# Kernel tuning notes

Hardware: AMD Instinct MI355X
Metric: run time of the kernel (lower is better)

Reference implementation:

```python
import jax, jax.numpy as jnp
import numpy as np


def setup_inputs() -> dict:
    key = jax.random.key(0)
    k1, k2 = jax.random.split(key)
    visual_features = jax.random.normal(k1, (16, 1024, 768), dtype=jnp.float32)
    text_tokens = jax.random.normal(k2, (16, 256, 768), dtype=jnp.float32)
    return {"visual_features": visual_features, "text_tokens": text_tokens, "k": 16}


def reference(visual_features, text_tokens, k):
    B, N, D = visual_features.shape
    T = min(k, N)

    # normalize (note: norm + 1e-6 in denominator, matching torch code)
    vis_norm = visual_features / (jnp.linalg.norm(visual_features, axis=-1, keepdims=True) + 1e-6)
    vis_norm = vis_norm.astype(jnp.float32)
    txt_norm = text_tokens / (jnp.linalg.norm(text_tokens, axis=-1, keepdims=True) + 1e-6)
    txt_norm = txt_norm.astype(jnp.float32)

    similarity = jnp.einsum('bnd,bmd->bnm', vis_norm, vis_norm)          # (B,N,N)
    relevance = jnp.einsum('bnd,btd->bnt', vis_norm, txt_norm).max(-1)    # (B,N)
    r_min = relevance.min(axis=1, keepdims=True)
    r_max = relevance.max(axis=1, keepdims=True)
    relevance = (relevance - r_min + 1e-6) / (r_max - r_min + 1e-6)

    kernel = relevance[:, :, None] * similarity * relevance[:, None, :]   # (B,N,N)

    di2s0 = jnp.diagonal(kernel, axis1=1, axis2=2)                        # (B,N)
    cis0 = jnp.zeros((T, B, N), dtype=kernel.dtype)
    barange = jnp.arange(B)

    def step(carry, i):
        di2s, cis = carry
        safe = jnp.maximum(di2s, 1e-12)
        j = jnp.argmax(safe, axis=-1)                                     # (B,)
        k_j = jnp.take_along_axis(kernel, j[:, None, None], axis=1)[:, 0, :]  # (B,N)
        dj = jnp.take_along_axis(di2s, j[:, None], axis=1)[:, 0]          # (B,)
        denom = jnp.sqrt(jnp.maximum(dj, 1e-12))[:, None] + 1e-8          # (B,1)
        # cis rows >= i are zero, so full-T contraction equals contraction over :i
        c_tb = jnp.take_along_axis(cis, j[None, :, None], axis=2)[:, :, 0]  # (T,B)
        cov = jnp.einsum('tb,tbn->bn', c_tb, cis)                         # (B,N)
        eis = (k_j - cov) / denom                                         # (B,N)
        cis = jax.lax.dynamic_update_index_in_dim(cis, eis, i, axis=0)
        di2s = di2s - eis ** 2
        di2s = di2s.at[barange, j].set(-jnp.inf)
        return (di2s, cis), j

    (_, _), sel = jax.lax.scan(step, (di2s0, cis0), jnp.arange(T))        # sel: (T,B)
    select_idx = jnp.sort(sel.T, axis=1)                                  # (B,T)
    selected = jnp.take_along_axis(visual_features, select_idx[:, :, None], axis=1)  # (B,T,D)
    if T < k:
        pad = jnp.zeros((B, k - T, D), dtype=selected.dtype)
        selected = jnp.concatenate([selected, pad], axis=1)
    return selected
```

## Files before the change

### kernel.cpp

```cpp
#include <hip/hip_runtime.h>
#include <math.h>

#define NB 16
#define NN 1024
#define ND 768
#define NT 256
#define NSEL 16
#define NC 64

typedef __attribute__((ext_vector_type(8))) short short8;
typedef __attribute__((ext_vector_type(4))) float f32x4;
typedef __attribute__((ext_vector_type(8))) unsigned short ushort8v;
typedef unsigned long long u64;

__device__ __align__(16) float g_invv[NB*NN];
__device__ __align__(16) float g_diagv[NB*NN];
__device__ __align__(16) float g_mrawp[NB*NN*2];
__device__ __align__(16) ushort8v g_tf[NB*2*24*2*8*64];

__device__ __forceinline__ unsigned short f2bf(float x) {
    unsigned u = __float_as_uint(x);
    return (unsigned short)((u + 0x7FFFu + ((u >> 16) & 1u)) >> 16);
}
__device__ __forceinline__ float bf2f(unsigned short h) {
    return __uint_as_float(((unsigned)h) << 16);
}
__device__ __forceinline__ size_t tfidx(int b, int th, int s, int h, int ct, int lane) {
    return ((((size_t)(b*2 + th)*24 + s)*2 + h)*8 + ct)*64 + lane;
}

__global__ __launch_bounds__(256) void ktxt(const float* __restrict__ txt) {
    int gw = (blockIdx.x * 256 + threadIdx.x) >> 6;
    int l  = threadIdx.x & 63;
    int b  = gw >> 8, r = gw & 255;
    int th = r >> 7, ct = (r >> 4) & 7, rlo = r & 15;
    const float* row = txt + (size_t)gw * ND;

    float4 x0 = *(const float4*)(row + 8*l);
    float4 y0 = *(const float4*)(row + 8*l + 4);
    float4 x1 = {0,0,0,0}, y1 = {0,0,0,0};
    bool two = (l < 32);
    if (two) {
        x1 = *(const float4*)(row + 512 + 8*l);
        y1 = *(const float4*)(row + 512 + 8*l + 4);
    }
    float s = x0.x*x0.x + x0.y*x0.y + x0.z*x0.z + x0.w*x0.w
            + y0.x*y0.x + y0.y*y0.y + y0.z*y0.z + y0.w*y0.w;
    if (two) s += x1.x*x1.x + x1.y*x1.y + x1.z*x1.z + x1.w*x1.w
                + y1.x*y1.x + y1.y*y1.y + y1.z*y1.z + y1.w*y1.w;
    #pragma unroll
    for (int off = 32; off; off >>= 1) s += __shfl_xor(s, off);
    float inv = 1.0f / (sqrtf(s) + 1e-6f);

    int kslot = l & 3;
    int lane  = kslot*16 + rlo;
    {
        int st = l >> 2;
        float a[8] = {x0.x, x0.y, x0.z, x0.w, y0.x, y0.y, y0.z, y0.w};
        ushort8v hh, ll;
        #pragma unroll
        for (int j = 0; j < 8; j++) {
            float v = a[j] * inv;
            hh[j] = f2bf(v);
            ll[j] = f2bf(v - bf2f(hh[j]));
        }
        g_tf[tfidx(b, th, st, 0, ct, lane)] = hh;
        g_tf[tfidx(b, th, st, 1, ct, lane)] = ll;
    }
    if (two) {
        int st = 16 + (l >> 2);
        float a[8] = {x1.x, x1.y, x1.z, x1.w, y1.x, y1.y, y1.z, y1.w};
        ushort8v hh, ll;
        #pragma unroll
        for (int j = 0; j < 8; j++) {
            float v = a[j] * inv;
            hh[j] = f2bf(v);
            ll[j] = f2bf(v - bf2f(hh[j]));
        }
        g_tf[tfidx(b, th, st, 0, ct, lane)] = hh;
        g_tf[tfidx(b, th, st, 1, ct, lane)] = ll;
    }
}

__global__ __launch_bounds__(256, 1) void krel(const float* __restrict__ vis) {
    int bid = blockIdx.x;
    int lid = (bid & 7) * 32 + (bid >> 3);
    int b   = lid >> 4;
    int r   = lid & 15;
    int mt  = r >> 1;
    int th  = r & 1;
    int t   = threadIdx.x;
    int w   = t >> 6, l = t & 63;

    f32x4 acc0[8], acc1[8];
    #pragma unroll
    for (int ct = 0; ct < 8; ct++) {
        acc0[ct] = (f32x4){0.f, 0.f, 0.f, 0.f};
        acc1[ct] = (f32x4){0.f, 0.f, 0.f, 0.f};
    }

    int base = mt*128 + w*32;
    const float* Ap0 = vis + ((size_t)(b*NN + base + (l & 15)))*ND + (l >> 4)*8;
    const float* Ap1 = Ap0 + (size_t)16*ND;

    const ushort8v* Bb = g_tf + (size_t)(b*2 + th)*(24*2*8*64) + l;

    float4 a0x = *(const float4*)(Ap0);
    float4 a0y = *(const float4*)(Ap0 + 4);
    float4 a1x = *(const float4*)(Ap1);
    float4 a1y = *(const float4*)(Ap1 + 4);
    float ss0 = 0.f, ss1 = 0.f;

    #define CONV8(AX, AY, AH, AL, SS)                                          \
        {                                                                      \
            float av_[8] = {AX.x, AX.y, AX.z, AX.w, AY.x, AY.y, AY.z, AY.w};   \
            ushort8v hh_, ll_;                                                 \
            _Pragma("unroll")                                                  \
            for (int j = 0; j < 8; j++) {                                      \
                hh_[j] = f2bf(av_[j]);                                         \
                ll_[j] = f2bf(av_[j] - bf2f(hh_[j]));                          \
                SS = fmaf(av_[j], av_[j], SS);                                 \
            }                                                                  \
            AH = *(short8*)&hh_;                                               \
            AL = *(short8*)&ll_;                                               \
        }

    #define MM(ACC, AA, BB)                                                    \
        _Pragma("unroll")                                                      \
        for (int ct = 0; ct < 8; ct++)                                         \
            ACC[ct] = __builtin_amdgcn_mfma_f32_16x16x32_bf16(                 \
                AA, *(short8*)&BB[ct], ACC[ct], 0, 0, 0);

    for (int s = 0; s < 24; s++) {
        const ushort8v* Bs = Bb + (size_t)s*(2*8*64);
        ushort8v bh[8], blv[8];
        #pragma unroll
        for (int ct = 0; ct < 8; ct++) {
            bh[ct]  = Bs[ct*64];
            blv[ct] = Bs[(8 + ct)*64];
        }
        float4 n0x, n0y, n1x, n1y;
        if (s < 23) {
            int k1 = (s + 1) * 32;
            n0x = *(const float4*)(Ap0 + k1);
            n0y = *(const float4*)(Ap0 + k1 + 4);
            n1x = *(const float4*)(Ap1 + k1);
            n1y = *(const float4*)(Ap1 + k1 + 4);
        }
        short8 ah0, al0, ah1, al1;
        CONV8(a0x, a0y, ah0, al0, ss0);
        CONV8(a1x, a1y, ah1, al1, ss1);
        MM(acc0, ah0, bh)  MM(acc0, al0, bh)  MM(acc0, ah0, blv)  MM(acc0, al0, blv)
        MM(acc1, ah1, bh)  MM(acc1, al1, bh)  MM(acc1, ah1, blv)  MM(acc1, al1, blv)
        if (s < 23) { a0x = n0x; a0y = n0y; a1x = n1x; a1y = n1y; }
        __builtin_amdgcn_s_barrier();
    }
    #undef MM
    #undef CONV8

    #define EPI(ACC, MOFF, SS)                                                 \
        {                                                                      \
            _Pragma("unroll")                                                  \
            for (int rr = 0; rr < 4; rr++) {                                   \
                float mx_ = ACC[0][rr];                                        \
                _Pragma("unroll")                                              \
                for (int ct = 1; ct < 8; ct++) mx_ = fmaxf(mx_, ACC[ct][rr]);  \
                _Pragma("unroll")                                              \
                for (int off = 1; off <= 8; off <<= 1)                         \
                    mx_ = fmaxf(mx_, __shfl_xor(mx_, off));                    \
                if ((l & 15) == 0)                                             \
                    g_mrawp[(size_t)(b*NN + base + (MOFF) + (l >> 4)*4 + rr)*2 + th] = mx_; \
            }                                                                  \
            float sst_ = SS;                                                   \
            sst_ += __shfl_xor(sst_, 16);                                      \
            sst_ += __shfl_xor(sst_, 32);                                      \
            if (th == 0 && l < 16) {                                           \
                int row_ = base + (MOFF) + l;                                  \
                float nrm_ = sqrtf(sst_);                                      \
                float inv_ = 1.0f / (nrm_ + 1e-6f);                            \
                g_invv[b*NN + row_] = inv_;                                    \
                float dd_ = nrm_ * inv_;                                       \
                g_diagv[b*NN + row_] = dd_ * dd_;                              \
            }                                                                  \
        }
    EPI(acc0, 0,  ss0)
    EPI(acc1, 16, ss1)
    #undef EPI
}

__global__ __launch_bounds__(1024) void kfinal(const float* __restrict__ vis,
                                               float* __restrict__ out) {
    int b = blockIdx.x;
    int t = threadIdx.x;
    int w = t >> 6, l = t & 63;

    __shared__ u64   s_key[NN];
    __shared__ float s_reln[NN];
    __shared__ __align__(16) unsigned short Chi[NC][392], Clo[NC][392];
    __shared__ float s_S[NC*65];
    __shared__ int   s_sel[NSEL], s_srt[NSEL];
    __shared__ float s_mn[16], s_mx[16], s_b2[2];

    float m0 = g_mrawp[(size_t)(b*NN + t)*2 + 0];
    float m1 = g_mrawp[(size_t)(b*NN + t)*2 + 1];
    float iv = g_invv[b*NN + t], dd = g_diagv[b*NN + t];
    float rr = fmaxf(m0, m1) * iv;
    float lmin = rr, lmax = rr;
    #pragma unroll
    for (int off = 32; off; off >>= 1) {
        lmin = fminf(lmin, __shfl_xor(lmin, off));
        lmax = fmaxf(lmax, __shfl_xor(lmax, off));
    }
    if (l == 0) { s_mn[w] = lmin; s_mx[w] = lmax; }
    __syncthreads();
    if (t == 0) {
        float mn = s_mn[0], mx = s_mx[0];
        #pragma unroll
        for (int q = 1; q < 16; q++) { mn = fminf(mn, s_mn[q]); mx = fmaxf(mx, s_mx[q]); }
        s_b2[0] = mn; s_b2[1] = mx;
    }
    __syncthreads();
    float mn = s_b2[0], mx = s_b2[1];
    float den = mx - mn + 1e-6f;
    float rn = (rr - mn + 1e-6f) / den;
    float d0 = rn * rn * dd;
    s_reln[t] = rn;
    u64 kreg = ((u64)(~__float_as_uint(d0)) << 10) | (unsigned)t;

    #pragma unroll
    for (int k = 2; k <= 64; k <<= 1) {
        #pragma unroll
        for (int j = k >> 1; j > 0; j >>= 1) {
            u64 part = __shfl_xor(kreg, j);
            bool takeMin = ((l & k) == 0) == ((l & j) == 0);
            kreg = takeMin ? (kreg < part ? kreg : part) : (kreg < part ? part : kreg);
        }
    }
    #pragma unroll
    for (int rnd = 0; rnd < 4; rnd++) {
        int dstp = 8 >> rnd;
        s_key[w*64 + l] = kreg;
        __syncthreads();
        u64 other = s_key[(w ^ dstp)*64 + (63 - l)];
        u64 m = (kreg < other) ? kreg : other;
        #pragma unroll
        for (int j = 32; j > 0; j >>= 1) {
            u64 part = __shfl_xor(m, j);
            bool takeMin = ((l & j) == 0);
            m = takeMin ? (m < part ? m : part) : (m < part ? part : m);
        }
        kreg = m;
        __syncthreads();
    }

    int   gid = (int)(kreg & 1023u);
    float d0v = __uint_as_float(~(unsigned)(kreg >> 10));

    f32x4 acc = (f32x4){0.f, 0.f, 0.f, 0.f};
    int ar0 = (w >> 2) * 16, bc0 = (w & 3) * 16;
    int cr  = (w << 2) + (l >> 4);
    int sgid = __shfl(gid, cr);
    float sc = g_invv[b*NN + sgid];
    const float* srcrow = vis + (size_t)(b*NN + sgid)*ND + (l & 15)*24;

    for (int c = 0; c < 2; c++) {
        __syncthreads();
        int kb = (l & 15) * 24;
        #pragma unroll
        for (int q = 0; q < 3; q++) {
            float4 x = *(const float4*)(srcrow + c*384 + q*8);
            float4 y = *(const float4*)(srcrow + c*384 + q*8 + 4);
            float av[8] = {x.x, x.y, x.z, x.w, y.x, y.y, y.z, y.w};
            ushort8v hh, ll;
            #pragma unroll
            for (int j = 0; j < 8; j++) {
                float vv = av[j] * sc;
                hh[j] = f2bf(vv);
                ll[j] = f2bf(vv - bf2f(hh[j]));
            }
            *(ushort8v*)&Chi[cr][kb + q*8] = hh;
            *(ushort8v*)&Clo[cr][kb + q*8] = ll;
        }
        __syncthreads();
        #pragma unroll
        for (int ks = 0; ks < 12; ks++) {
            int ko = ks*32 + (l >> 4)*8;
            short8 ah = *(const short8*)&Chi[ar0 + (l & 15)][ko];
            short8 al = *(const short8*)&Clo[ar0 + (l & 15)][ko];
            short8 bh = *(const short8*)&Chi[bc0 + (l & 15)][ko];
            short8 bl = *(const short8*)&Clo[bc0 + (l & 15)][ko];
            acc = __builtin_amdgcn_mfma_f32_16x16x32_bf16(ah, bh, acc, 0, 0, 0);
            acc = __builtin_amdgcn_mfma_f32_16x16x32_bf16(al, bh, acc, 0, 0, 0);
            acc = __builtin_amdgcn_mfma_f32_16x16x32_bf16(ah, bl, acc, 0, 0, 0);
            acc = __builtin_amdgcn_mfma_f32_16x16x32_bf16(al, bl, acc, 0, 0, 0);
        }
    }
    #pragma unroll
    for (int r = 0; r < 4; r++)
        s_S[(ar0 + (l >> 4)*4 + r)*65 + bc0 + (l & 15)] = acc[r];
    __syncthreads();

    if (w == 0) {
        float di  = d0v;
        int   gd  = gid;
        float rel = s_reln[gid];
        float ownc[NSEL];
        #pragma unroll
        for (int i = 0; i < NSEL; i++) {
            float vq = fmaxf(di, 1e-12f);
            int   gq = gd;
            int   cq = l;
            #pragma unroll
            for (int off = 32; off; off >>= 1) {
                float vo = __shfl_xor(vq, off);
                int   go = __shfl_xor(gq, off);
                int   co = __shfl_xor(cq, off);
                if (vo > vq || (vo == vq && go < gq)) { vq = vo; gq = go; cq = co; }
            }
            float dj   = __shfl(di, cq);
            float relj = __shfl(rel, cq);
            float denom = sqrtf(fmaxf(dj, 1e-12f)) + 1e-8f;
            if (l == 0) s_sel[i] = gq;

            float cov = 0.f;
            #pragma unroll
            for (int q = 0; q < i; q++)
                cov = fmaf(ownc[q], __shfl(ownc[q], cq), cov);

            float sim = s_S[l*65 + cq];
            float kj  = rel * relj * sim;
            float eis = (kj - cov) / denom;
            ownc[i] = eis;
            di = di - eis * eis;
            if (l == cq) di = -__builtin_inff();
        }
    }
    __syncthreads();

    if (t == 0) {
        int vv[16];
        #pragma unroll
        for (int q = 0; q < 16; q++) vv[q] = s_sel[q];
        for (int a = 1; a < 16; a++) {
            int key = vv[a]; int p2 = a - 1;
            while (p2 >= 0 && vv[p2] > key) { vv[p2+1] = vv[p2]; p2--; }
            vv[p2+1] = key;
        }
        #pragma unroll
        for (int q = 0; q < 16; q++) s_srt[q] = vv[q];
    }
    __syncthreads();
    {
        int idx = s_srt[w];
        const float* src = vis + (size_t)(b*NN + idx)*ND + l*12;
        float*       dst = out + (size_t)(b*NSEL + w)*ND + l*12;
        float4 x = *(const float4*)(src);
        float4 y = *(const float4*)(src + 4);
        float4 z = *(const float4*)(src + 8);
        *(float4*)(dst)     = x;
        *(float4*)(dst + 4) = y;
        *(float4*)(dst + 8) = z;
    }
}

extern "C" void kernel_launch(void* const* d_in, const int* in_sizes, int n_in,
                              void* d_out, int out_size, void* d_ws, size_t ws_size,
                              hipStream_t stream) {
    (void)in_sizes; (void)n_in; (void)d_ws; (void)ws_size; (void)out_size;
    const float* vis = (const float*)d_in[0];
    const float* txt = (const float*)d_in[1];
    float* out = (float*)d_out;

    ktxt  <<<dim3((NB*NT)/4), dim3(256),  0, stream>>>(txt);
    krel  <<<dim3(256),       dim3(256),  0, stream>>>(vis);
    kfinal<<<dim3(NB),        dim3(1024), 0, stream>>>(vis, out);
}
```

Before: 82.00 us.

## Stage B fragments in LDS via async triple-buffered loads in krel

Result: slower. 88.52 us (+8.0%).

```diff
diff --git a/kernel.cpp b/kernel.cpp
--- a/kernel.cpp
+++ b/kernel.cpp
@@ -82,15 +82,17 @@
     }
 }
 
-__global__ __launch_bounds__(256, 1) void krel(const float* __restrict__ vis) {
+__global__ __launch_bounds__(128, 1) void krel(const float* __restrict__ vis) {
     int bid = blockIdx.x;
-    int lid = (bid & 7) * 32 + (bid >> 3);
-    int b   = lid >> 4;
-    int r   = lid & 15;
-    int mt  = r >> 1;
+    int lid = (bid & 7) * 64 + (bid >> 3);
+    int b   = lid >> 5;
+    int r   = lid & 31;
     int th  = r & 1;
+    int blk = r >> 1;
     int t   = threadIdx.x;
     int w   = t >> 6, l = t & 63;
+
+    __shared__ __align__(16) ushort8v Bfrag[3][2][8][64];
 
     f32x4 acc0[8], acc1[8];
     #pragma unroll
@@ -99,64 +101,91 @@
         acc1[ct] = (f32x4){0.f, 0.f, 0.f, 0.f};
     }
 
-    int base = mt*128 + w*32;
+    int base = blk*64 + w*32;
     const float* Ap0 = vis + ((size_t)(b*NN + base + (l & 15)))*ND + (l >> 4)*8;
     const float* Ap1 = Ap0 + (size_t)16*ND;
 
-    const ushort8v* Bb = g_tf + (size_t)(b*2 + th)*(24*2*8*64) + l;
+    const ushort8v* Bbase = g_tf + (size_t)(b*2 + th)*(24*2*8*64);
+
+    #define STAGE(S, P)                                                          \
+        {                                                                        \
+            _Pragma("unroll")                                                    \
+            for (int q = 0; q < 8; q++) {                                        \
+                int c  = w*8 + q;                                                \
+                int h  = c >> 3, ct = c & 7;                                     \
+                const ushort8v* gsrc = Bbase + (((size_t)(S)*2 + h)*8 + ct)*64 + l; \
+                __builtin_amdgcn_global_load_lds(                                \
+                    (const __attribute__((address_space(1))) void*)gsrc,         \
+                    (__attribute__((address_space(3))) void*)&Bfrag[P][h][ct][0],\
+                    16, 0, 0);                                                   \
+            }                                                                    \
+        }
 
     float4 a0x = *(const float4*)(Ap0);
     float4 a0y = *(const float4*)(Ap0 + 4);
     float4 a1x = *(const float4*)(Ap1);
     float4 a1y = *(const float4*)(Ap1 + 4);
+    STAGE(0, 0);
+    STAGE(1, 1);
+    __syncthreads();
     float ss0 = 0.f, ss1 = 0.f;
 
-    #define CONV8(AX, AY, AH, AL, SS)                                          \
-        {                                                                      \
-            float av_[8] = {AX.x, AX.y, AX.z, AX.w, AY.x, AY.y, AY.z, AY.w};   \
-            ushort8v hh_, ll_;                                                 \
-            _Pragma("unroll")                                                  \
-            for (int j = 0; j < 8; j++) {                                      \
-                hh_[j] = f2bf(av_[j]);                                         \
-                ll_[j] = f2bf(av_[j] - bf2f(hh_[j]));                          \
-                SS = fmaf(av_[j], av_[j], SS);                                 \
-            }                                                                  \
-            AH = *(short8*)&hh_;                                               \
-            AL = *(short8*)&ll_;                                               \
-        }
-
-    #define MM(ACC, AA, BB)                                                    \
-        _Pragma("unroll")                                                      \
-        for (int ct = 0; ct < 8; ct++)                                         \
-            ACC[ct] = __builtin_amdgcn_mfma_f32_16x16x32_bf16(                 \
-                AA, *(short8*)&BB[ct], ACC[ct], 0, 0, 0);
-
     for (int s = 0; s < 24; s++) {
-        const ushort8v* Bs = Bb + (size_t)s*(2*8*64);
-        ushort8v bh[8], blv[8];
-        #pragma unroll
-        for (int ct = 0; ct < 8; ct++) {
-            bh[ct]  = Bs[ct*64];
-            blv[ct] = Bs[(8 + ct)*64];
-        }
-        float4 n0x, n0y, n1x, n1y;
+        int p = s % 3;
+        if (s < 22) STAGE(s + 2, (s + 2) % 3);
+        asm volatile("" ::: "memory");
+        short8 ah0, al0, ah1, al1;
+        {
+            float av[8] = {a0x.x, a0x.y, a0x.z, a0x.w, a0y.x, a0y.y, a0y.z, a0y.w};
+            ushort8v hh, ll;
+            #pragma unroll
+            for (int j = 0; j < 8; j++) {
+                hh[j] = f2bf(av[j]);
+                ll[j] = f2bf(av[j] - bf2f(hh[j]));
+                ss0 = fmaf(av[j], av[j], ss0);
+            }
+            ah0 = *(short8*)&hh; al0 = *(short8*)&ll;
+        }
+        {
+            float av[8] = {a1x.x, a1x.y, a1x.z, a1x.w, a1y.x, a1y.y, a1y.z, a1y.w};
+            ushort8v hh, ll;
+            #pragma unroll
+            for (int j = 0; j < 8; j++) {
+                hh[j] = f2bf(av[j]);
+                ll[j] = f2bf(av[j] - bf2f(hh[j]));
+                ss1 = fmaf(av[j], av[j], ss1);
+            }
+            ah1 = *(short8*)&hh; al1 = *(short8*)&ll;
+        }
         if (s < 23) {
             int k1 = (s + 1) * 32;
-            n0x = *(const float4*)(Ap0 + k1);
-            n0y = *(const float4*)(Ap0 + k1 + 4);
-            n1x = *(const float4*)(Ap1 + k1);
-            n1y = *(const float4*)(Ap1 + k1 + 4);
-        }
-        short8 ah0, al0, ah1, al1;
-        CONV8(a0x, a0y, ah0, al0, ss0);
-        CONV8(a1x, a1y, ah1, al1, ss1);
-        MM(acc0, ah0, bh)  MM(acc0, al0, bh)  MM(acc0, ah0, blv)  MM(acc0, al0, blv)
-        MM(acc1, ah1, bh)  MM(acc1, al1, bh)  MM(acc1, ah1, blv)  MM(acc1, al1, blv)
-        if (s < 23) { a0x = n0x; a0y = n0y; a1x = n1x; a1y = n1y; }
-        __builtin_amdgcn_s_barrier();
-    }
-    #undef MM
-    #undef CONV8
+            a0x = *(const float4*)(Ap0 + k1);
+            a0y = *(const float4*)(Ap0 + k1 + 4);
+            a1x = *(const float4*)(Ap1 + k1);
+            a1y = *(const float4*)(Ap1 + k1 + 4);
+        }
+        __builtin_amdgcn_s_setprio(1);
+        #pragma unroll
+        for (int ct = 0; ct < 8; ct++) {
+            short8 bh = *(const short8*)&Bfrag[p][0][ct][l];
+            short8 bl = *(const short8*)&Bfrag[p][1][ct][l];
+            acc0[ct] = __builtin_amdgcn_mfma_f32_16x16x32_bf16(ah0, bh, acc0[ct], 0, 0, 0);
+            acc0[ct] = __builtin_amdgcn_mfma_f32_16x16x32_bf16(al0, bh, acc0[ct], 0, 0, 0);
+            acc0[ct] = __builtin_amdgcn_mfma_f32_16x16x32_bf16(ah0, bl, acc0[ct], 0, 0, 0);
+            acc0[ct] = __builtin_amdgcn_mfma_f32_16x16x32_bf16(al0, bl, acc0[ct], 0, 0, 0);
+            acc1[ct] = __builtin_amdgcn_mfma_f32_16x16x32_bf16(ah1, bh, acc1[ct], 0, 0, 0);
+            acc1[ct] = __builtin_amdgcn_mfma_f32_16x16x32_bf16(al1, bh, acc1[ct], 0, 0, 0);
+            acc1[ct] = __builtin_amdgcn_mfma_f32_16x16x32_bf16(ah1, bl, acc1[ct], 0, 0, 0);
+            acc1[ct] = __builtin_amdgcn_mfma_f32_16x16x32_bf16(al1, bl, acc1[ct], 0, 0, 0);
+        }
+        __builtin_amdgcn_s_setprio(0);
+        if (s < 23) {
+            asm volatile("s_waitcnt lgkmcnt(0)" ::: "memory");
+            __builtin_amdgcn_s_barrier();
+            __builtin_amdgcn_sched_barrier(0);
+        }
+    }
+    #undef STAGE
 
     #define EPI(ACC, MOFF, SS)                                                 \
         {                                                                      \
@@ -372,6 +401,6 @@
     float* out = (float*)d_out;
 
     ktxt  <<<dim3((NB*NT)/4), dim3(256),  0, stream>>>(txt);
-    krel  <<<dim3(256),       dim3(256),  0, stream>>>(vis);
+    krel  <<<dim3(512),       dim3(128),  0, stream>>>(vis);
     kfinal<<<dim3(NB),        dim3(1024), 0, stream>>>(vis, out);
 }
```
